# Kernel tuning notes

Hardware: AMD Instinct MI355X
Metric: run time of the kernel (lower is better)

The kernel has to match this reference:

```python
import jax, jax.numpy as jnp
import numpy as np

N_QUBITS = 6
N_QLAYERS = 3
CNOT = jnp.array([[1,0,0,0],[0,1,0,0],[0,0,0,1],[0,0,1,0]], dtype=jnp.complex64).reshape(2,2,2,2)


def _rx(t):
    c = jnp.cos(0.5 * t).astype(jnp.complex64)
    s = jnp.sin(0.5 * t).astype(jnp.complex64)
    return jnp.stack([jnp.stack([c, -1j * s]), jnp.stack([-1j * s, c])])


def _ry(t):
    c = jnp.cos(0.5 * t).astype(jnp.complex64)
    s = jnp.sin(0.5 * t).astype(jnp.complex64)
    return jnp.stack([jnp.stack([c, -s]), jnp.stack([s, c])])


def _rz(t):
    e0 = jnp.exp(-0.5j * t)
    e1 = jnp.exp(0.5j * t)
    z = jnp.zeros((), jnp.complex64)
    return jnp.stack([jnp.stack([e0, z]), jnp.stack([z, e1])])


def _apply1(state, U, wire):
    st = jnp.tensordot(U, state, axes=([1], [wire]))
    return jnp.moveaxis(st, 0, wire)


def _apply_cnot(state, c, t):
    st = jnp.tensordot(CNOT, state, axes=([2, 3], [c, t]))
    return jnp.moveaxis(st, (0, 1), (c, t))


def _circuit(inputs, weights):
    # 6-qubit statevector sim of the PennyLane circuit; inputs: [6], weights: [3,6]
    state = jnp.zeros((2,) * N_QUBITS, jnp.complex64).at[(0,) * N_QUBITS].set(1.0)
    for i in range(N_QUBITS):
        state = _apply1(state, _rx(inputs[i % N_QUBITS]), i)
        state = _apply1(state, _ry(inputs[(i + 1) % N_QUBITS]), i)
        state = _apply1(state, _rz(inputs[(i + 2) % N_QUBITS]), i)
    for _l in range(N_QLAYERS):
        for q in range(N_QUBITS):
            state = _apply1(state, _ry(weights[_l, q]), q)
        for q in range(N_QUBITS):
            state = _apply_cnot(state, q, (q + 1) % N_QUBITS)
    probs = jnp.abs(state) ** 2
    zvec = jnp.array([1.0, -1.0], jnp.float32)
    return jnp.stack([jnp.tensordot(probs, zvec, axes=([i], [0])).sum() for i in range(N_QUBITS)])


def _forward(x, cw1, cb1, cw2, cb2, cw3, cb3, W_ih, W_hh, b_ih, b_hh, q_weights, Wq, bq, Wo, bo):
    h = jnp.transpose(x, (0, 2, 1))  # [B, F, T]
    for W, b in ((cw1, cb1), (cw2, cb2), (cw3, cb3)):
        h = jax.lax.conv_general_dilated(h, W, (1,), [(1, 1)], dimension_numbers=('NCH', 'OIH', 'NCH')) + b[None, :, None]
        h = jax.nn.relu(h)
    tcn_out = jnp.transpose(h, (0, 2, 1))  # [B, T, H]
    B, H = x.shape[0], tcn_out.shape[2]
    qbatch = jax.vmap(lambda inp: _circuit(inp, q_weights))

    def step(carry, x_t):
        hx, cx = carry
        gates = x_t @ W_ih.T + b_ih + hx @ W_hh.T + b_hh
        i_g, f_g, g_g, o_g = jnp.split(gates, 4, axis=1)
        c = jax.nn.sigmoid(f_g) * cx + jax.nn.sigmoid(i_g) * jnp.tanh(g_g)
        hh = jax.nn.sigmoid(o_g) * jnp.tanh(c)
        hh = 3.99 * hh * (1.0 - hh)  # logistic map
        x_new = 1.0 - 1.4 * hh[:, 0] ** 2 + hh[:, 1]  # henon map on dims 0,1
        y_new = 0.3 * hh[:, 0]
        hh = jnp.concatenate([x_new[:, None], y_new[:, None], hh[:, 2:]], axis=1)
        q = qbatch(hh[:, :N_QUBITS])  # [B, 6]
        hh = hh + q @ Wq.T + bq  # QuantumRNNCell(hx, hx)
        return (hh, c), None

    step = jax.checkpoint(step)
    hx = jnp.zeros((B, H), x.dtype)
    cx = jnp.zeros((B, H), x.dtype)
    (hx, cx), _ = jax.lax.scan(step, (hx, cx), jnp.swapaxes(tcn_out, 0, 1))
    return jax.nn.sigmoid(hx @ Wo.T + bo)  # [B, 1]


def setup_inputs() -> dict:
    key = jax.random.key(0)
    ks = jax.random.split(key, 20)
    B, T, F, H = 4096, 256, 32, 32

    def u(k, shape, fan):
        s = 1.0 / np.sqrt(fan)
        return jax.random.uniform(k, shape, jnp.float32, -s, s)

    return {
        'x': jax.random.normal(ks[0], (B, T, F), jnp.float32),
        'cw1': u(ks[1], (H, F, 3), F * 3), 'cb1': u(ks[2], (H,), F * 3),
        'cw2': u(ks[3], (H, H, 3), H * 3), 'cb2': u(ks[4], (H,), H * 3),
        'cw3': u(ks[5], (H, H, 3), H * 3), 'cb3': u(ks[6], (H,), H * 3),
        'W_ih': u(ks[7], (4 * H, H), H), 'W_hh': u(ks[8], (4 * H, H), H),
        'b_ih': u(ks[9], (4 * H,), H), 'b_hh': u(ks[10], (4 * H,), H),
        'q_weights': jax.random.uniform(ks[11], (N_QLAYERS, N_QUBITS), jnp.float32, 0.0, 2.0 * np.pi),
        'Wq': u(ks[12], (H, N_QUBITS), N_QUBITS), 'bq': u(ks[13], (H,), N_QUBITS),
        'Wo': u(ks[14], (1, H), H), 'bo': u(ks[15], (1,), H),
    }


def reference(x, cw1, cb1, cw2, cb2, cw3, cb3, W_ih, W_hh, b_ih, b_hh, q_weights, Wq, bq, Wo, bo):
    return _forward(x, cw1, cb1, cw2, cb2, cw3, cb3, W_ih, W_hh, b_ih, b_hh, q_weights, Wq, bq, Wo, bo)
```

## Files before the change

### kernel.cpp

```cpp
#include <hip/hip_runtime.h>

#define B_TOT 4096
#define T_LEN 256
#define NCH   32

typedef float f2 __attribute__((ext_vector_type(2)));
typedef float f4 __attribute__((ext_vector_type(4)));

__device__ __forceinline__ float rdlane(float v, int l) {
    return __int_as_float(__builtin_amdgcn_readlane(__float_as_int(v), l));
}
__device__ __forceinline__ float xor1f(float x) {
    return __int_as_float(__builtin_amdgcn_mov_dpp(__float_as_int(x), 0xB1, 0xF, 0xF, true));
}
__device__ __forceinline__ float xor2f(float x) {
    return __int_as_float(__builtin_amdgcn_mov_dpp(__float_as_int(x), 0x4E, 0xF, 0xF, true));
}
__device__ __forceinline__ float xor3f(float x) {
    return __int_as_float(__builtin_amdgcn_mov_dpp(__float_as_int(x), 0x1B, 0xF, 0xF, true));
}
__device__ __forceinline__ float xsign(float x, unsigned m) {
    return __int_as_float(__float_as_int(x) ^ (int)m);
}
__device__ __forceinline__ float fast_sig(float x) {
    return __builtin_amdgcn_rcpf(1.0f + __expf(-x));
}
__device__ __forceinline__ float fast_tanh(float x) {
    return fmaf(-2.0f, __builtin_amdgcn_rcpf(__expf(2.0f * x) + 1.0f), 1.0f);
}

__device__ __forceinline__ void fast_sincos(float x, float& s, float& c) {
    float k = rintf(x * 0.3183098861837907f);
    float r = fmaf(-k, 3.14159274101257324f, x);
    r = fmaf(-k, -8.74227765734758577e-8f, r);
    float r2 = r * r;
    float sp = -2.50521084e-8f;
    sp = fmaf(sp, r2, 2.75573192e-6f);
    sp = fmaf(sp, r2, -1.98412698e-4f);
    sp = fmaf(sp, r2, 8.33333333e-3f);
    sp = fmaf(sp, r2, -1.66666667e-1f);
    float sv = fmaf(sp * r2, r, r);
    float cp = 2.08767570e-9f;
    cp = fmaf(cp, r2, -2.75573192e-7f);
    cp = fmaf(cp, r2, 2.48015873e-5f);
    cp = fmaf(cp, r2, -1.38888889e-3f);
    cp = fmaf(cp, r2, 4.16666667e-2f);
    cp = fmaf(cp, r2, -0.5f);
    float cv = fmaf(cp, r2, 1.0f);
    float sgn = ((int)k & 1) ? -1.0f : 1.0f;
    s = sv * sgn;
    c = cv * sgn;
}

__global__ __launch_bounds__(256) void tcn_kernel(
    const float* __restrict__ x,
    const float* __restrict__ cw1, const float* __restrict__ cb1,
    const float* __restrict__ cw2, const float* __restrict__ cb2,
    const float* __restrict__ cw3, const float* __restrict__ cb3,
    float* __restrict__ out)
{
    __shared__ float bufA[NCH * 257];
    __shared__ float bufB[NCH * 257];
    __shared__ float sW[NCH * 97];
    __shared__ float sB[NCH];

    const int b   = blockIdx.x;
    const int tid = threadIdx.x;
    const float* xb = x + (size_t)b * T_LEN * NCH;

    #pragma unroll
    for (int c = 0; c < 32; ++c) {
        int idx = c * 256 + tid;
        int t = idx >> 5, f = idx & 31;
        bufA[f * 257 + t] = xb[idx];
    }
    __syncthreads();

    float* bin  = bufA;
    float* bout = bufB;
    const int o  = tid & 31;
    const int t0 = (tid >> 5) * 32;

    for (int layer = 0; layer < 3; ++layer) {
        const float* Wg = (layer == 0) ? cw1 : ((layer == 1) ? cw2 : cw3);
        const float* Bg = (layer == 0) ? cb1 : ((layer == 1) ? cb2 : cb3);
        for (int idx = tid; idx < 32 * 96; idx += 256) {
            int oo = idx / 96, rem = idx - oo * 96;
            sW[oo * 97 + rem] = Wg[idx];
        }
        if (tid < 32) sB[tid] = Bg[tid];
        __syncthreads();

        float acc[32];
        const float bias = sB[o];
        #pragma unroll
        for (int tt = 0; tt < 32; ++tt) acc[tt] = bias;

        for (int i = 0; i < 32; ++i) {
            const float w0 = sW[o * 97 + i * 3 + 0];
            const float w1 = sW[o * 97 + i * 3 + 1];
            const float w2 = sW[o * 97 + i * 3 + 2];
            const float* row = bin + i * 257;
            float vm = (t0 == 0) ? 0.0f : row[t0 - 1];
            float v0 = row[t0];
            #pragma unroll
            for (int tt = 0; tt < 32; ++tt) {
                float vp = (t0 + tt == 255) ? 0.0f : row[t0 + tt + 1];
                acc[tt] = fmaf(w0, vm, acc[tt]);
                acc[tt] = fmaf(w1, v0, acc[tt]);
                acc[tt] = fmaf(w2, vp, acc[tt]);
                vm = v0; v0 = vp;
            }
        }
        #pragma unroll
        for (int tt = 0; tt < 32; ++tt)
            bout[o * 257 + t0 + tt] = fmaxf(acc[tt], 0.0f);
        __syncthreads();
        float* tmp = bin; bin = bout; bout = tmp;
    }

    float* og = out + (size_t)b * T_LEN * NCH;
    #pragma unroll
    for (int c = 0; c < 32; ++c) {
        int idx = c * 256 + tid;
        int t = idx >> 5, f = idx & 31;
        og[idx] = bin[f * 257 + t];
    }
}

__global__ __launch_bounds__(64) void scan_kernel(
    const float* __restrict__ tcn,
    const float* __restrict__ W_ih, const float* __restrict__ W_hh,
    const float* __restrict__ b_ih, const float* __restrict__ b_hh,
    const float* __restrict__ qw,
    const float* __restrict__ Wq, const float* __restrict__ bq,
    const float* __restrict__ Wo, const float* __restrict__ bo,
    float* __restrict__ out)
{
    __shared__ __align__(16) float xc2[64];
    __shared__ __align__(16) float colb[24];

    const int lane = threadIdx.x;
    const int b    = blockIdx.x;
    const float* xrow = tcn + (size_t)b * T_LEN * NCH;

    f2 wih[32], whh[32];
    #pragma unroll
    for (int k = 0; k < 32; ++k) {
        wih[k] = f2{ W_ih[lane * 32 + k], W_ih[(lane + 64) * 32 + k] };
        whh[k] = f2{ W_hh[lane * 32 + k], W_hh[(lane + 64) * 32 + k] };
    }
    const f2 bias01 = f2{ b_ih[lane] + b_hh[lane],
                          b_ih[lane + 64] + b_hh[lane + 64] };

    float ssu[18], ccu[18];
    {
        float s0, c0;
        int j = (lane < 18) ? lane : 0;
        fast_sincos(0.5f * qw[j], s0, c0);
        #pragma unroll
        for (int i = 0; i < 18; ++i) { ssu[i] = rdlane(s0, i); ccu[i] = rdlane(c0, i); }
    }
    float vs1 = ssu[0], vc1 = ccu[0];
    #pragma unroll
    for (int i = 1; i < 6; ++i) {
        vs1 = (lane == i) ? ssu[i] : vs1;
        vc1 = (lane == i) ? ccu[i] : vc1;
    }
    const int MU2[6] = {31, 48, 56, 60, 62, 63};
    const int MU3[6] = {53, 47, 23, 43, 21, 42};
    float ssl2[6], ssl3[6], cc2[6], cc3[6];
    #pragma unroll
    for (int q = 0; q < 6; ++q) {
        ssl2[q] = (__popc(lane & MU2[q]) & 1) ? ssu[6 + q]  : -ssu[6 + q];
        ssl3[q] = (__popc(lane & MU3[q]) & 1) ? ssu[12 + q] : -ssu[12 + q];
        cc2[q] = ccu[6 + q];
        cc3[q] = ccu[12 + q];
    }
    unsigned nm[6];
    #pragma unroll
    for (int q = 0; q < 6; ++q) nm[q] = (lane & (32 >> q)) ? 0u : 0x80000000u;
    int cidx[6];
    #pragma unroll
    for (int i = 0; i < 6; ++i) cidx[i] = i * 2 + ((lane & (32 >> i)) ? 1 : 0);
    const int r1 = (lane + 1) % 6, r2 = (lane + 2) % 6;

    float wqr[6] = {0, 0, 0, 0, 0, 0};
    float bqr = 0.0f, wor = 0.0f;
    if (lane < 32) {
        #pragma unroll
        for (int k = 0; k < 6; ++k) wqr[k] = Wq[lane * 6 + k];
        bqr = bq[lane];
        wor = Wo[lane];
    }

    float hh = 0.0f, cxs = 0.0f;
    float xpre = (lane < 32) ? xrow[lane] : 0.0f;
    const f4* xcq  = (const f4*)xc2;
    const f2* colq = (const f2*)colb;

    for (int t = 0; t < T_LEN; ++t) {
        if (lane < 32) ((f2*)xc2)[lane] = f2{xpre, hh};
        float xnext = (lane < 32 && t < T_LEN - 1) ? xrow[(t + 1) * 32 + lane] : 0.0f;

        f2 acc = bias01, accb = f2{0.0f, 0.0f};
        #pragma unroll
        for (int j = 0; j < 16; ++j) {
            f4 v = xcq[j];
            acc  = __builtin_elementwise_fma(wih[2 * j],     __builtin_shufflevector(v, v, 0, 0), acc);
            acc  = __builtin_elementwise_fma(whh[2 * j],     __builtin_shufflevector(v, v, 1, 1), acc);
            accb = __builtin_elementwise_fma(wih[2 * j + 1], __builtin_shufflevector(v, v, 2, 2), accb);
            accb = __builtin_elementwise_fma(whh[2 * j + 1], __builtin_shufflevector(v, v, 3, 3), accb);
        }
        acc += accb;
        float acc0 = acc.x, acc1 = acc.y;

        float fg = __shfl_xor(acc0, 32, 64);
        float og = __shfl_xor(acc1, 32, 64);
        float c  = fast_sig(fg) * cxs + fast_sig(acc0) * fast_tanh(acc1);
        float h  = fast_sig(og) * fast_tanh(c);
        h = 3.99f * h * (1.0f - h);
        float h0 = rdlane(h, 0), h1 = rdlane(h, 1);
        float hen0 = fmaf(-1.4f * h0, h0, 1.0f) + h1;
        float hen1 = 0.3f * h0;
        h = (lane == 0) ? hen0 : h;
        h = (lane == 1) ? hen1 : h;
        cxs = c;

        float s_own, c_own;
        fast_sincos(0.5f * h, s_own, c_own);
        float s1v = __shfl(s_own, r1, 64), c1v = __shfl(c_own, r1, 64);
        float s2v = __shfl(s_own, r2, 64), c2v = __shfl(c_own, r2, 64);
        float A_ = c1v * c_own, Bv = s1v * s_own;
        float C_ = s1v * c_own, D_ = c1v * s_own;
        float ur = fmaf(Bv, s2v,  A_ * c2v);
        float ui = fmaf(Bv, c2v, -(A_ * s2v));
        float pr = fmaf(D_, s2v,  C_ * c2v);
        float pi = fmaf(C_, s2v, -(D_ * c2v));
        float nur = fmaf(vc1, ur, -(vs1 * pr));
        float nui = fmaf(vc1, ui, -(vs1 * pi));
        float npr = fmaf(vs1, ur,  vc1 * pr);
        float npi = fmaf(vs1, ui,  vc1 * pi);
        if (lane < 6) *(f4*)&colb[lane * 4] = f4{nur, nui, npr, npi};

        f2 g0 = colq[cidx[0]];
        float re = g0.x, im = g0.y;
        #pragma unroll
        for (int i = 1; i < 6; ++i) {
            f2 g = colq[cidx[i]];
            float nr = fmaf(re, g.x, -(im * g.y));
            float ni = fmaf(re, g.y,   im * g.x);
            re = nr; im = ni;
        }

        {
            float pre, pim;
            pre = __shfl_xor(re, 48, 64); pim = __shfl_xor(im, 48, 64);
            re = fmaf(ssl2[0], pre, cc2[0] * re); im = fmaf(ssl2[0], pim, cc2[0] * im);
            pre = __shfl_xor(re, 24, 64); pim = __shfl_xor(im, 24, 64);
            re = fmaf(ssl2[1], pre, cc2[1] * re); im = fmaf(ssl2[1], pim, cc2[1] * im);
            pre = __shfl_xor(re, 12, 64); pim = __shfl_xor(im, 12, 64);
            re = fmaf(ssl2[2], pre, cc2[2] * re); im = fmaf(ssl2[2], pim, cc2[2] * im);
            pre = __shfl_xor(re, 6, 64);  pim = __shfl_xor(im, 6, 64);
            re = fmaf(ssl2[3], pre, cc2[3] * re); im = fmaf(ssl2[3], pim, cc2[3] * im);
            pre = xor3f(re);              pim = xor3f(im);
            re = fmaf(ssl2[4], pre, cc2[4] * re); im = fmaf(ssl2[4], pim, cc2[4] * im);
            pre = __shfl_xor(re, 49, 64); pim = __shfl_xor(im, 49, 64);
            re = fmaf(ssl2[5], pre, cc2[5] * re); im = fmaf(ssl2[5], pim, cc2[5] * im);
        }
        {
            float pre, pim;
            pre = __shfl_xor(re, 40, 64); pim = __shfl_xor(im, 40, 64);
            re = fmaf(ssl3[0], pre, cc3[0] * re); im = fmaf(ssl3[0], pim, cc3[0] * im);
            pre = __shfl_xor(re, 20, 64); pim = __shfl_xor(im, 20, 64);
            re = fmaf(ssl3[1], pre, cc3[1] * re); im = fmaf(ssl3[1], pim, cc3[1] * im);
            pre = __shfl_xor(re, 10, 64); pim = __shfl_xor(im, 10, 64);
            re = fmaf(ssl3[2], pre, cc3[2] * re); im = fmaf(ssl3[2], pim, cc3[2] * im);
            pre = __shfl_xor(re, 5, 64);  pim = __shfl_xor(im, 5, 64);
            re = fmaf(ssl3[3], pre, cc3[3] * re); im = fmaf(ssl3[3], pim, cc3[3] * im);
            pre = __shfl_xor(re, 50, 64); pim = __shfl_xor(im, 50, 64);
            re = fmaf(ssl3[4], pre, cc3[4] * re); im = fmaf(ssl3[4], pim, cc3[4] * im);
            pre = __shfl_xor(re, 25, 64); pim = __shfl_xor(im, 25, 64);
            re = fmaf(ssl3[5], pre, cc3[5] * re); im = fmaf(ssl3[5], pim, cc3[5] * im);
        }

        float p = fmaf(re, re, im * im);
        { float pp = xor1f(p);               p = pp - xsign(p, nm[5]); }
        { float pp = xor2f(p);               p = pp - xsign(p, nm[4]); }
        { float pp = __shfl_xor(p, 4, 64);   p = pp - xsign(p, nm[3]); }
        { float pp = __shfl_xor(p, 8, 64);   p = pp - xsign(p, nm[2]); }
        { float pp = __shfl_xor(p, 16, 64);  p = pp - xsign(p, nm[1]); }
        { float pp = __shfl_xor(p, 32, 64);  p = pp - xsign(p, nm[0]); }

        float upd = bqr;
        upd = fmaf(rdlane(p, 44), wqr[0], upd);
        upd = fmaf(rdlane(p, 26), wqr[1], upd);
        upd = fmaf(rdlane(p, 13), wqr[2], upd);
        upd = fmaf(rdlane(p, 38), wqr[3], upd);
        upd = fmaf(rdlane(p, 51), wqr[4], upd);
        upd = fmaf(rdlane(p, 25), wqr[5], upd);
        hh = h + upd;
        xpre = xnext;
    }

    float contrib = (lane < 32) ? hh * wor : 0.0f;
    #pragma unroll
    for (int off = 32; off >= 1; off >>= 1)
        contrib += __shfl_xor(contrib, off, 64);
    if (lane == 0) out[b] = fast_sig(contrib + bo[0]);
}

extern "C" void kernel_launch(void* const* d_in, const int* in_sizes, int n_in,
                              void* d_out, int out_size, void* d_ws, size_t ws_size,
                              hipStream_t stream)
{
    const float* x    = (const float*)d_in[0];
    const float* cw1  = (const float*)d_in[1];
    const float* cb1  = (const float*)d_in[2];
    const float* cw2  = (const float*)d_in[3];
    const float* cb2  = (const float*)d_in[4];
    const float* cw3  = (const float*)d_in[5];
    const float* cb3  = (const float*)d_in[6];
    const float* W_ih = (const float*)d_in[7];
    const float* W_hh = (const float*)d_in[8];
    const float* b_ih = (const float*)d_in[9];
    const float* b_hh = (const float*)d_in[10];
    const float* qw   = (const float*)d_in[11];
    const float* Wq   = (const float*)d_in[12];
    const float* bq   = (const float*)d_in[13];
    const float* Wo   = (const float*)d_in[14];
    const float* bo   = (const float*)d_in[15];

    float* tcn = (float*)d_ws;

    hipLaunchKernelGGL(tcn_kernel, dim3(B_TOT), dim3(256), 0, stream,
                       x, cw1, cb1, cw2, cb2, cw3, cb3, tcn);
    hipLaunchKernelGGL(scan_kernel, dim3(B_TOT), dim3(64), 0, stream,
                       tcn, W_ih, W_hh, b_ih, b_hh, qw, Wq, bq, Wo, bo,
                       (float*)d_out);
}
```

Baseline: 1.113 ms.

## Interleave two sequences per scan wavefront and vectorize TCN conv with f2

The scan kernel now handles two batch rows per 64-lane block, interleaving the LSTM, quantum-circuit and reduction chains of both so their latencies overlap, and launches half as many blocks. The quantum angle sincos drops range reduction (sincos_poly) because the inputs are bounded. One shuffle is replaced by a DPP row move. The TCN conv pads rows to 258 for 8-byte alignment and uses packed f2 FMAs. The extra register pressure from two interleaved states may lower occupancy, and the unreduced polynomial assumes small arguments.

Measured after the change: 996.4 us, median of 3. -10.5%, faster.

```diff
diff --git a/kernel.cpp b/kernel.cpp
--- a/kernel.cpp
+++ b/kernel.cpp
@@ -18,6 +18,9 @@
 }
 __device__ __forceinline__ float xor3f(float x) {
     return __int_as_float(__builtin_amdgcn_mov_dpp(__float_as_int(x), 0x1B, 0xF, 0xF, true));
+}
+__device__ __forceinline__ float xor8f(float x) {
+    return __int_as_float(__builtin_amdgcn_mov_dpp(__float_as_int(x), 0x128, 0xF, 0xF, true));
 }
 __device__ __forceinline__ float xsign(float x, unsigned m) {
     return __int_as_float(__float_as_int(x) ^ (int)m);
@@ -34,14 +37,12 @@
     float r = fmaf(-k, 3.14159274101257324f, x);
     r = fmaf(-k, -8.74227765734758577e-8f, r);
     float r2 = r * r;
-    float sp = -2.50521084e-8f;
-    sp = fmaf(sp, r2, 2.75573192e-6f);
+    float sp = fmaf(-2.50521084e-8f, r2, 2.75573192e-6f);
     sp = fmaf(sp, r2, -1.98412698e-4f);
     sp = fmaf(sp, r2, 8.33333333e-3f);
     sp = fmaf(sp, r2, -1.66666667e-1f);
     float sv = fmaf(sp * r2, r, r);
-    float cp = 2.08767570e-9f;
-    cp = fmaf(cp, r2, -2.75573192e-7f);
+    float cp = fmaf(2.08767570e-9f, r2, -2.75573192e-7f);
     cp = fmaf(cp, r2, 2.48015873e-5f);
     cp = fmaf(cp, r2, -1.38888889e-3f);
     cp = fmaf(cp, r2, 4.16666667e-2f);
@@ -52,6 +53,21 @@
     c = cv * sgn;
 }
 
+__device__ __forceinline__ void sincos_poly(float x, float& s, float& c) {
+    float r2 = x * x;
+    float sp = fmaf(-2.50521084e-8f, r2, 2.75573192e-6f);
+    sp = fmaf(sp, r2, -1.98412698e-4f);
+    sp = fmaf(sp, r2, 8.33333333e-3f);
+    sp = fmaf(sp, r2, -1.66666667e-1f);
+    s = fmaf(sp * r2, x, x);
+    float cp = fmaf(2.08767570e-9f, r2, -2.75573192e-7f);
+    cp = fmaf(cp, r2, 2.48015873e-5f);
+    cp = fmaf(cp, r2, -1.38888889e-3f);
+    cp = fmaf(cp, r2, 4.16666667e-2f);
+    cp = fmaf(cp, r2, -0.5f);
+    c = fmaf(cp, r2, 1.0f);
+}
+
 __global__ __launch_bounds__(256) void tcn_kernel(
     const float* __restrict__ x,
     const float* __restrict__ cw1, const float* __restrict__ cb1,
@@ -59,8 +75,8 @@
     const float* __restrict__ cw3, const float* __restrict__ cb3,
     float* __restrict__ out)
 {
-    __shared__ float bufA[NCH * 257];
-    __shared__ float bufB[NCH * 257];
+    __shared__ float bufA[NCH * 258];
+    __shared__ float bufB[NCH * 258];
     __shared__ float sW[NCH * 97];
     __shared__ float sB[NCH];
 
@@ -72,7 +88,7 @@
     for (int c = 0; c < 32; ++c) {
         int idx = c * 256 + tid;
         int t = idx >> 5, f = idx & 31;
-        bufA[f * 257 + t] = xb[idx];
+        bufA[f * 258 + t] = xb[idx];
     }
     __syncthreads();
 
@@ -91,30 +107,41 @@
         if (tid < 32) sB[tid] = Bg[tid];
         __syncthreads();
 
-        float acc[32];
+        f2 acc2[16];
         const float bias = sB[o];
         #pragma unroll
-        for (int tt = 0; tt < 32; ++tt) acc[tt] = bias;
+        for (int j = 0; j < 16; ++j) acc2[j] = f2{bias, bias};
 
         for (int i = 0; i < 32; ++i) {
             const float w0 = sW[o * 97 + i * 3 + 0];
             const float w1 = sW[o * 97 + i * 3 + 1];
             const float w2 = sW[o * 97 + i * 3 + 2];
-            const float* row = bin + i * 257;
-            float vm = (t0 == 0) ? 0.0f : row[t0 - 1];
-            float v0 = row[t0];
+            const float* row = bin + i * 258;
+            const f2* rp = (const f2*)(row + t0);
+            float vmE = (t0 == 0)   ? 0.0f : row[t0 - 1];
+            float vpE = (t0 == 224) ? 0.0f : row[t0 + 32];
+            f2 Lprev = f2{0.0f, 0.0f};
+            f2 Lcur  = rp[0];
             #pragma unroll
-            for (int tt = 0; tt < 32; ++tt) {
-                float vp = (t0 + tt == 255) ? 0.0f : row[t0 + tt + 1];
-                acc[tt] = fmaf(w0, vm, acc[tt]);
-                acc[tt] = fmaf(w1, v0, acc[tt]);
-                acc[tt] = fmaf(w2, vp, acc[tt]);
-                vm = v0; v0 = vp;
+            for (int j = 0; j < 16; ++j) {
+                f2 Lnext = (j < 15) ? rp[j + 1] : f2{vpE, 0.0f};
+                f2 vm = (j == 0) ? f2{vmE, Lcur.x}
+                                 : __builtin_shufflevector(Lprev, Lcur, 1, 2);
+                f2 vp = __builtin_shufflevector(Lcur, Lnext, 1, 2);
+                acc2[j] = __builtin_elementwise_fma(f2{w0, w0}, vm,   acc2[j]);
+                acc2[j] = __builtin_elementwise_fma(f2{w1, w1}, Lcur, acc2[j]);
+                acc2[j] = __builtin_elementwise_fma(f2{w2, w2}, vp,   acc2[j]);
+                Lprev = Lcur; Lcur = Lnext;
             }
         }
-        #pragma unroll
-        for (int tt = 0; tt < 32; ++tt)
-            bout[o * 257 + t0 + tt] = fmaxf(acc[tt], 0.0f);
+        f2* wout = (f2*)(bout + o * 258 + t0);
+        #pragma unroll
+        for (int j = 0; j < 16; ++j) {
+            f2 r;
+            r.x = fmaxf(acc2[j].x, 0.0f);
+            r.y = fmaxf(acc2[j].y, 0.0f);
+            wout[j] = r;
+        }
         __syncthreads();
         float* tmp = bin; bin = bout; bout = tmp;
     }
@@ -124,11 +151,11 @@
     for (int c = 0; c < 32; ++c) {
         int idx = c * 256 + tid;
         int t = idx >> 5, f = idx & 31;
-        og[idx] = bin[f * 257 + t];
-    }
-}
-
-__global__ __launch_bounds__(64) void scan_kernel(
+        og[idx] = bin[f * 258 + t];
+    }
+}
+
+__global__ __launch_bounds__(64, 2) void scan_kernel(
     const float* __restrict__ tcn,
     const float* __restrict__ W_ih, const float* __restrict__ W_hh,
     const float* __restrict__ b_ih, const float* __restrict__ b_hh,
@@ -137,12 +164,13 @@
     const float* __restrict__ Wo, const float* __restrict__ bo,
     float* __restrict__ out)
 {
-    __shared__ __align__(16) float xc2[64];
-    __shared__ __align__(16) float colb[24];
+    __shared__ __align__(16) float xcA[64], xcB[64];
+    __shared__ __align__(16) float colA[24], colB[24];
 
     const int lane = threadIdx.x;
-    const int b    = blockIdx.x;
-    const float* xrow = tcn + (size_t)b * T_LEN * NCH;
+    const int b2   = blockIdx.x * 2;
+    const float* xrowA = tcn + (size_t)b2 * T_LEN * NCH;
+    const float* xrowB = xrowA + T_LEN * NCH;
 
     f2 wih[32], whh[32];
     #pragma unroll
@@ -194,120 +222,200 @@
         wor = Wo[lane];
     }
 
-    float hh = 0.0f, cxs = 0.0f;
-    float xpre = (lane < 32) ? xrow[lane] : 0.0f;
-    const f4* xcq  = (const f4*)xc2;
-    const f2* colq = (const f2*)colb;
+    float hhA = 0.0f, cellA = 0.0f, hhB = 0.0f, cellB = 0.0f;
+    float xpA = (lane < 32) ? xrowA[lane] : 0.0f;
+    float xpB = (lane < 32) ? xrowB[lane] : 0.0f;
+
+    const f4* xqA = (const f4*)xcA;
+    const f4* xqB = (const f4*)xcB;
+    const f2* clA = (const f2*)colA;
+    const f2* clB = (const f2*)colB;
 
     for (int t = 0; t < T_LEN; ++t) {
-        if (lane < 32) ((f2*)xc2)[lane] = f2{xpre, hh};
-        float xnext = (lane < 32 && t < T_LEN - 1) ? xrow[(t + 1) * 32 + lane] : 0.0f;
-
-        f2 acc = bias01, accb = f2{0.0f, 0.0f};
+        if (lane < 32) {
+            ((f2*)xcA)[lane] = f2{xpA, hhA};
+            ((f2*)xcB)[lane] = f2{xpB, hhB};
+        }
+        float xnA = (lane < 32 && t < T_LEN - 1) ? xrowA[(t + 1) * 32 + lane] : 0.0f;
+        float xnB = (lane < 32 && t < T_LEN - 1) ? xrowB[(t + 1) * 32 + lane] : 0.0f;
+
+        f2 aA = bias01, bA_ = f2{0.0f, 0.0f};
+        f2 aB = bias01, bB_ = f2{0.0f, 0.0f};
         #pragma unroll
         for (int j = 0; j < 16; ++j) {
-            f4 v = xcq[j];
-            acc  = __builtin_elementwise_fma(wih[2 * j],     __builtin_shufflevector(v, v, 0, 0), acc);
-            acc  = __builtin_elementwise_fma(whh[2 * j],     __builtin_shufflevector(v, v, 1, 1), acc);
-            accb = __builtin_elementwise_fma(wih[2 * j + 1], __builtin_shufflevector(v, v, 2, 2), accb);
-            accb = __builtin_elementwise_fma(whh[2 * j + 1], __builtin_shufflevector(v, v, 3, 3), accb);
-        }
-        acc += accb;
-        float acc0 = acc.x, acc1 = acc.y;
-
-        float fg = __shfl_xor(acc0, 32, 64);
-        float og = __shfl_xor(acc1, 32, 64);
-        float c  = fast_sig(fg) * cxs + fast_sig(acc0) * fast_tanh(acc1);
-        float h  = fast_sig(og) * fast_tanh(c);
-        h = 3.99f * h * (1.0f - h);
-        float h0 = rdlane(h, 0), h1 = rdlane(h, 1);
-        float hen0 = fmaf(-1.4f * h0, h0, 1.0f) + h1;
-        float hen1 = 0.3f * h0;
-        h = (lane == 0) ? hen0 : h;
-        h = (lane == 1) ? hen1 : h;
-        cxs = c;
-
-        float s_own, c_own;
-        fast_sincos(0.5f * h, s_own, c_own);
-        float s1v = __shfl(s_own, r1, 64), c1v = __shfl(c_own, r1, 64);
-        float s2v = __shfl(s_own, r2, 64), c2v = __shfl(c_own, r2, 64);
-        float A_ = c1v * c_own, Bv = s1v * s_own;
-        float C_ = s1v * c_own, D_ = c1v * s_own;
-        float ur = fmaf(Bv, s2v,  A_ * c2v);
-        float ui = fmaf(Bv, c2v, -(A_ * s2v));
-        float pr = fmaf(D_, s2v,  C_ * c2v);
-        float pi = fmaf(C_, s2v, -(D_ * c2v));
-        float nur = fmaf(vc1, ur, -(vs1 * pr));
-        float nui = fmaf(vc1, ui, -(vs1 * pi));
-        float npr = fmaf(vs1, ur,  vc1 * pr);
-        float npi = fmaf(vs1, ui,  vc1 * pi);
-        if (lane < 6) *(f4*)&colb[lane * 4] = f4{nur, nui, npr, npi};
-
-        f2 g0 = colq[cidx[0]];
-        float re = g0.x, im = g0.y;
+            f4 vA = xqA[j], vB = xqB[j];
+            aA  = __builtin_elementwise_fma(wih[2*j],   __builtin_shufflevector(vA, vA, 0, 0), aA);
+            aB  = __builtin_elementwise_fma(wih[2*j],   __builtin_shufflevector(vB, vB, 0, 0), aB);
+            aA  = __builtin_elementwise_fma(whh[2*j],   __builtin_shufflevector(vA, vA, 1, 1), aA);
+            aB  = __builtin_elementwise_fma(whh[2*j],   __builtin_shufflevector(vB, vB, 1, 1), aB);
+            bA_ = __builtin_elementwise_fma(wih[2*j+1], __builtin_shufflevector(vA, vA, 2, 2), bA_);
+            bB_ = __builtin_elementwise_fma(wih[2*j+1], __builtin_shufflevector(vB, vB, 2, 2), bB_);
+            bA_ = __builtin_elementwise_fma(whh[2*j+1], __builtin_shufflevector(vA, vA, 3, 3), bA_);
+            bB_ = __builtin_elementwise_fma(whh[2*j+1], __builtin_shufflevector(vB, vB, 3, 3), bB_);
+        }
+        aA += bA_; aB += bB_;
+        float acc0A = aA.x, acc1A = aA.y;
+        float acc0B = aB.x, acc1B = aB.y;
+
+        float fgA = __shfl_xor(acc0A, 32, 64), ogA = __shfl_xor(acc1A, 32, 64);
+        float fgB = __shfl_xor(acc0B, 32, 64), ogB = __shfl_xor(acc1B, 32, 64);
+        float cA = fast_sig(fgA) * cellA + fast_sig(acc0A) * fast_tanh(acc1A);
+        float cB = fast_sig(fgB) * cellB + fast_sig(acc0B) * fast_tanh(acc1B);
+        float hA = fast_sig(ogA) * fast_tanh(cA);
+        float hB = fast_sig(ogB) * fast_tanh(cB);
+        hA = 3.99f * hA * (1.0f - hA);
+        hB = 3.99f * hB * (1.0f - hB);
+        float h0A = rdlane(hA, 0), h1A = rdlane(hA, 1);
+        float h0B = rdlane(hB, 0), h1B = rdlane(hB, 1);
+        float henA0 = fmaf(-1.4f * h0A, h0A, 1.0f) + h1A;
+        float henB0 = fmaf(-1.4f * h0B, h0B, 1.0f) + h1B;
+        hA = (lane == 0) ? henA0 : hA;
+        hB = (lane == 0) ? henB0 : hB;
+        hA = (lane == 1) ? 0.3f * h0A : hA;
+        hB = (lane == 1) ? 0.3f * h0B : hB;
+        cellA = cA; cellB = cB;
+
+        float sOA, cOA, sOB, cOB;
+        sincos_poly(0.5f * hA, sOA, cOA);
+        sincos_poly(0.5f * hB, sOB, cOB);
+        float s1A = __shfl(sOA, r1, 64), c1A = __shfl(cOA, r1, 64);
+        float s1B = __shfl(sOB, r1, 64), c1B = __shfl(cOB, r1, 64);
+        float s2A = __shfl(sOA, r2, 64), c2A = __shfl(cOA, r2, 64);
+        float s2B = __shfl(sOB, r2, 64), c2B = __shfl(cOB, r2, 64);
+        {
+            float A_ = c1A * cOA, Bv = s1A * sOA;
+            float C_ = s1A * cOA, D_ = c1A * sOA;
+            float ur = fmaf(Bv, s2A,  A_ * c2A);
+            float ui = fmaf(Bv, c2A, -(A_ * s2A));
+            float pr = fmaf(D_, s2A,  C_ * c2A);
+            float pi = fmaf(C_, s2A, -(D_ * c2A));
+            float nur = fmaf(vc1, ur, -(vs1 * pr));
+            float nui = fmaf(vc1, ui, -(vs1 * pi));
+            float npr = fmaf(vs1, ur,  vc1 * pr);
+            float npi = fmaf(vs1, ui,  vc1 * pi);
+            if (lane < 6) *(f4*)&colA[lane * 4] = f4{nur, nui, npr, npi};
+        }
+        {
+            float A_ = c1B * cOB, Bv = s1B * sOB;
+            float C_ = s1B * cOB, D_ = c1B * sOB;
+            float ur = fmaf(Bv, s2B,  A_ * c2B);
+            float ui = fmaf(Bv, c2B, -(A_ * s2B));
+            float pr = fmaf(D_, s2B,  C_ * c2B);
+            float pi = fmaf(C_, s2B, -(D_ * c2B));
+            float nur = fmaf(vc1, ur, -(vs1 * pr));
+            float nui = fmaf(vc1, ui, -(vs1 * pi));
+            float npr = fmaf(vs1, ur,  vc1 * pr);
+            float npi = fmaf(vs1, ui,  vc1 * pi);
+            if (lane < 6) *(f4*)&colB[lane * 4] = f4{nur, nui, npr, npi};
+        }
+
+        f2 gA0 = clA[cidx[0]], gB0 = clB[cidx[0]];
+        float reA = gA0.x, imA = gA0.y;
+        float reB = gB0.x, imB = gB0.y;
         #pragma unroll
         for (int i = 1; i < 6; ++i) {
-            f2 g = colq[cidx[i]];
-            float nr = fmaf(re, g.x, -(im * g.y));
-            float ni = fmaf(re, g.y,   im * g.x);
-            re = nr; im = ni;
+            f2 gA = clA[cidx[i]], gB = clB[cidx[i]];
+            float nrA = fmaf(reA, gA.x, -(imA * gA.y));
+            float niA = fmaf(reA, gA.y,   imA * gA.x);
+            float nrB = fmaf(reB, gB.x, -(imB * gB.y));
+            float niB = fmaf(reB, gB.y,   imB * gB.x);
+            reA = nrA; imA = niA; reB = nrB; imB = niB;
         }
 
         {
-            float pre, pim;
-            pre = __shfl_xor(re, 48, 64); pim = __shfl_xor(im, 48, 64);
-            re = fmaf(ssl2[0], pre, cc2[0] * re); im = fmaf(ssl2[0], pim, cc2[0] * im);
-            pre = __shfl_xor(re, 24, 64); pim = __shfl_xor(im, 24, 64);
-            re = fmaf(ssl2[1], pre, cc2[1] * re); im = fmaf(ssl2[1], pim, cc2[1] * im);
-            pre = __shfl_xor(re, 12, 64); pim = __shfl_xor(im, 12, 64);
-            re = fmaf(ssl2[2], pre, cc2[2] * re); im = fmaf(ssl2[2], pim, cc2[2] * im);
-            pre = __shfl_xor(re, 6, 64);  pim = __shfl_xor(im, 6, 64);
-            re = fmaf(ssl2[3], pre, cc2[3] * re); im = fmaf(ssl2[3], pim, cc2[3] * im);
-            pre = xor3f(re);              pim = xor3f(im);
-            re = fmaf(ssl2[4], pre, cc2[4] * re); im = fmaf(ssl2[4], pim, cc2[4] * im);
-            pre = __shfl_xor(re, 49, 64); pim = __shfl_xor(im, 49, 64);
-            re = fmaf(ssl2[5], pre, cc2[5] * re); im = fmaf(ssl2[5], pim, cc2[5] * im);
+            float pA, qA, pB, qB;
+            pA = __shfl_xor(reA, 48, 64); qA = __shfl_xor(imA, 48, 64);
+            pB = __shfl_xor(reB, 48, 64); qB = __shfl_xor(imB, 48, 64);
+            reA = fmaf(ssl2[0], pA, cc2[0] * reA); imA = fmaf(ssl2[0], qA, cc2[0] * imA);
+            reB = fmaf(ssl2[0], pB, cc2[0] * reB); imB = fmaf(ssl2[0], qB, cc2[0] * imB);
+            pA = __shfl_xor(reA, 24, 64); qA = __shfl_xor(imA, 24, 64);
+            pB = __shfl_xor(reB, 24, 64); qB = __shfl_xor(imB, 24, 64);
+            reA = fmaf(ssl2[1], pA, cc2[1] * reA); imA = fmaf(ssl2[1], qA, cc2[1] * imA);
+            reB = fmaf(ssl2[1], pB, cc2[1] * reB); imB = fmaf(ssl2[1], qB, cc2[1] * imB);
+            pA = __shfl_xor(reA, 12, 64); qA = __shfl_xor(imA, 12, 64);
+            pB = __shfl_xor(reB, 12, 64); qB = __shfl_xor(imB, 12, 64);
+            reA = fmaf(ssl2[2], pA, cc2[2] * reA); imA = fmaf(ssl2[2], qA, cc2[2] * imA);
+            reB = fmaf(ssl2[2], pB, cc2[2] * reB); imB = fmaf(ssl2[2], qB, cc2[2] * imB);
+            pA = __shfl_xor(reA, 6, 64);  qA = __shfl_xor(imA, 6, 64);
+            pB = __shfl_xor(reB, 6, 64);  qB = __shfl_xor(imB, 6, 64);
+            reA = fmaf(ssl2[3], pA, cc2[3] * reA); imA = fmaf(ssl2[3], qA, cc2[3] * imA);
+            reB = fmaf(ssl2[3], pB, cc2[3] * reB); imB = fmaf(ssl2[3], qB, cc2[3] * imB);
+            pA = xor3f(reA); qA = xor3f(imA);
+            pB = xor3f(reB); qB = xor3f(imB);
+            reA = fmaf(ssl2[4], pA, cc2[4] * reA); imA = fmaf(ssl2[4], qA, cc2[4] * imA);
+            reB = fmaf(ssl2[4], pB, cc2[4] * reB); imB = fmaf(ssl2[4], qB, cc2[4] * imB);
+            pA = __shfl_xor(reA, 49, 64); qA = __shfl_xor(imA, 49, 64);
+            pB = __shfl_xor(reB, 49, 64); qB = __shfl_xor(imB, 49, 64);
+            reA = fmaf(ssl2[5], pA, cc2[5] * reA); imA = fmaf(ssl2[5], qA, cc2[5] * imA);
+            reB = fmaf(ssl2[5], pB, cc2[5] * reB); imB = fmaf(ssl2[5], qB, cc2[5] * imB);
         }
         {
-            float pre, pim;
-            pre = __shfl_xor(re, 40, 64); pim = __shfl_xor(im, 40, 64);
-            re = fmaf(ssl3[0], pre, cc3[0] * re); im = fmaf(ssl3[0], pim, cc3[0] * im);
-            pre = __shfl_xor(re, 20, 64); pim = __shfl_xor(im, 20, 64);
-            re = fmaf(ssl3[1], pre, cc3[1] * re); im = fmaf(ssl3[1], pim, cc3[1] * im);
-            pre = __shfl_xor(re, 10, 64); pim = __shfl_xor(im, 10, 64);
-            re = fmaf(ssl3[2], pre, cc3[2] * re); im = fmaf(ssl3[2], pim, cc3[2] * im);
-            pre = __shfl_xor(re, 5, 64);  pim = __shfl_xor(im, 5, 64);
-            re = fmaf(ssl3[3], pre, cc3[3] * re); im = fmaf(ssl3[3], pim, cc3[3] * im);
-            pre = __shfl_xor(re, 50, 64); pim = __shfl_xor(im, 50, 64);
-            re = fmaf(ssl3[4], pre, cc3[4] * re); im = fmaf(ssl3[4], pim, cc3[4] * im);
-            pre = __shfl_xor(re, 25, 64); pim = __shfl_xor(im, 25, 64);
-            re = fmaf(ssl3[5], pre, cc3[5] * re); im = fmaf(ssl3[5], pim, cc3[5] * im);
-        }
-
-        float p = fmaf(re, re, im * im);
-        { float pp = xor1f(p);               p = pp - xsign(p, nm[5]); }
-        { float pp = xor2f(p);               p = pp - xsign(p, nm[4]); }
-        { float pp = __shfl_xor(p, 4, 64);   p = pp - xsign(p, nm[3]); }
-        { float pp = __shfl_xor(p, 8, 64);   p = pp - xsign(p, nm[2]); }
-        { float pp = __shfl_xor(p, 16, 64);  p = pp - xsign(p, nm[1]); }
-        { float pp = __shfl_xor(p, 32, 64);  p = pp - xsign(p, nm[0]); }
-
-        float upd = bqr;
-        upd = fmaf(rdlane(p, 44), wqr[0], upd);
-        upd = fmaf(rdlane(p, 26), wqr[1], upd);
-        upd = fmaf(rdlane(p, 13), wqr[2], upd);
-        upd = fmaf(rdlane(p, 38), wqr[3], upd);
-        upd = fmaf(rdlane(p, 51), wqr[4], upd);
-        upd = fmaf(rdlane(p, 25), wqr[5], upd);
-        hh = h + upd;
-        xpre = xnext;
-    }
-
-    float contrib = (lane < 32) ? hh * wor : 0.0f;
-    #pragma unroll
-    for (int off = 32; off >= 1; off >>= 1)
-        contrib += __shfl_xor(contrib, off, 64);
-    if (lane == 0) out[b] = fast_sig(contrib + bo[0]);
+            float pA, qA, pB, qB;
+            pA = __shfl_xor(reA, 40, 64); qA = __shfl_xor(imA, 40, 64);
+            pB = __shfl_xor(reB, 40, 64); qB = __shfl_xor(imB, 40, 64);
+            reA = fmaf(ssl3[0], pA, cc3[0] * reA); imA = fmaf(ssl3[0], qA, cc3[0] * imA);
+            reB = fmaf(ssl3[0], pB, cc3[0] * reB); imB = fmaf(ssl3[0], qB, cc3[0] * imB);
+            pA = __shfl_xor(reA, 20, 64); qA = __shfl_xor(imA, 20, 64);
+            pB = __shfl_xor(reB, 20, 64); qB = __shfl_xor(imB, 20, 64);
+            reA = fmaf(ssl3[1], pA, cc3[1] * reA); imA = fmaf(ssl3[1], qA, cc3[1] * imA);
+            reB = fmaf(ssl3[1], pB, cc3[1] * reB); imB = fmaf(ssl3[1], qB, cc3[1] * imB);
+            pA = __shfl_xor(reA, 10, 64); qA = __shfl_xor(imA, 10, 64);
+            pB = __shfl_xor(reB, 10, 64); qB = __shfl_xor(imB, 10, 64);
+            reA = fmaf(ssl3[2], pA, cc3[2] * reA); imA = fmaf(ssl3[2], qA, cc3[2] * imA);
+            reB = fmaf(ssl3[2], pB, cc3[2] * reB); imB = fmaf(ssl3[2], qB, cc3[2] * imB);
+            pA = __shfl_xor(reA, 5, 64);  qA = __shfl_xor(imA, 5, 64);
+            pB = __shfl_xor(reB, 5, 64);  qB = __shfl_xor(imB, 5, 64);
+            reA = fmaf(ssl3[3], pA, cc3[3] * reA); imA = fmaf(ssl3[3], qA, cc3[3] * imA);
+            reB = fmaf(ssl3[3], pB, cc3[3] * reB); imB = fmaf(ssl3[3], qB, cc3[3] * imB);
+            pA = __shfl_xor(reA, 50, 64); qA = __shfl_xor(imA, 50, 64);
+            pB = __shfl_xor(reB, 50, 64); qB = __shfl_xor(imB, 50, 64);
+            reA = fmaf(ssl3[4], pA, cc3[4] * reA); imA = fmaf(ssl3[4], qA, cc3[4] * imA);
+            reB = fmaf(ssl3[4], pB, cc3[4] * reB); imB = fmaf(ssl3[4], qB, cc3[4] * imB);
+            pA = __shfl_xor(reA, 25, 64); qA = __shfl_xor(imA, 25, 64);
+            pB = __shfl_xor(reB, 25, 64); qB = __shfl_xor(imB, 25, 64);
+            reA = fmaf(ssl3[5], pA, cc3[5] * reA); imA = fmaf(ssl3[5], qA, cc3[5] * imA);
+            reB = fmaf(ssl3[5], pB, cc3[5] * reB); imB = fmaf(ssl3[5], qB, cc3[5] * imB);
+        }
+
+        float pA = fmaf(reA, reA, imA * imA);
+        float pB = fmaf(reB, reB, imB * imB);
+        { float tA = xor1f(pA), tB = xor1f(pB);
+          pA = tA - xsign(pA, nm[5]); pB = tB - xsign(pB, nm[5]); }
+        { float tA = xor2f(pA), tB = xor2f(pB);
+          pA = tA - xsign(pA, nm[4]); pB = tB - xsign(pB, nm[4]); }
+        { float tA = __shfl_xor(pA, 4, 64), tB = __shfl_xor(pB, 4, 64);
+          pA = tA - xsign(pA, nm[3]); pB = tB - xsign(pB, nm[3]); }
+        { float tA = xor8f(pA), tB = xor8f(pB);
+          pA = tA - xsign(pA, nm[2]); pB = tB - xsign(pB, nm[2]); }
+        { float tA = __shfl_xor(pA, 16, 64), tB = __shfl_xor(pB, 16, 64);
+          pA = tA - xsign(pA, nm[1]); pB = tB - xsign(pB, nm[1]); }
+        { float tA = __shfl_xor(pA, 32, 64), tB = __shfl_xor(pB, 32, 64);
+          pA = tA - xsign(pA, nm[0]); pB = tB - xsign(pB, nm[0]); }
+
+        float updA = bqr, updB = bqr;
+        updA = fmaf(rdlane(pA, 44), wqr[0], updA); updB = fmaf(rdlane(pB, 44), wqr[0], updB);
+        updA = fmaf(rdlane(pA, 26), wqr[1], updA); updB = fmaf(rdlane(pB, 26), wqr[1], updB);
+        updA = fmaf(rdlane(pA, 13), wqr[2], updA); updB = fmaf(rdlane(pB, 13), wqr[2], updB);
+        updA = fmaf(rdlane(pA, 38), wqr[3], updA); updB = fmaf(rdlane(pB, 38), wqr[3], updB);
+        updA = fmaf(rdlane(pA, 51), wqr[4], updA); updB = fmaf(rdlane(pB, 51), wqr[4], updB);
+        updA = fmaf(rdlane(pA, 25), wqr[5], updA); updB = fmaf(rdlane(pB, 25), wqr[5], updB);
+        hhA = hA + updA;
+        hhB = hB + updB;
+        xpA = xnA; xpB = xnB;
+    }
+
+    float cA = (lane < 32) ? hhA * wor : 0.0f;
+    float cB = (lane < 32) ? hhB * wor : 0.0f;
+    #pragma unroll
+    for (int off = 32; off >= 1; off >>= 1) {
+        cA += __shfl_xor(cA, off, 64);
+        cB += __shfl_xor(cB, off, 64);
+    }
+    if (lane == 0) {
+        float bo0 = bo[0];
+        out[b2]     = fast_sig(cA + bo0);
+        out[b2 + 1] = fast_sig(cB + bo0);
+    }
 }
 
 extern "C" void kernel_launch(void* const* d_in, const int* in_sizes, int n_in,
@@ -335,7 +443,7 @@
 
     hipLaunchKernelGGL(tcn_kernel, dim3(B_TOT), dim3(256), 0, stream,
                        x, cw1, cb1, cw2, cb2, cw3, cb3, tcn);
-    hipLaunchKernelGGL(scan_kernel, dim3(B_TOT), dim3(64), 0, stream,
+    hipLaunchKernelGGL(scan_kernel, dim3(B_TOT / 2), dim3(64), 0, stream,
                        tcn, W_ih, W_hh, b_ih, b_hh, qw, Wq, bq, Wo, bo,
                        (float*)d_out);
 }
```
